# Performance work log

Measured on AMD Instinct MI355X. Metric: run time of the kernel, lower is better.

Reference implementation:

```python
import jax, jax.numpy as jnp
import numpy as np

NUM_HEADS = 4
CHUNK = 64
GATE_NORM = 16.0
EPS = 1e-5


def _xavier(key, fan_in, fan_out):
    gain = 2.0 ** (-2.5)
    limit = gain * np.sqrt(6.0 / (fan_in + fan_out))
    return jax.random.uniform(key, (fan_in, fan_out), jnp.float32, -limit, limit)


def setup_inputs() -> dict:
    key = jax.random.key(0)
    ks = jax.random.split(key, 8)
    B, L, D = 4, 2048, 1024
    Dk, Dv, R = 1024, 2048, 16
    x = jax.random.normal(ks[0], (B, L, D), jnp.float32)
    return {
        "x": x,
        "Wq": _xavier(ks[1], D, Dk),
        "Wk": _xavier(ks[2], D, Dk),
        "Wv": _xavier(ks[3], D, Dv),
        "Wg": _xavier(ks[4], D, Dv),
        "gk_w1": _xavier(ks[5], D, R),
        "gk_w2": _xavier(ks[6], R, Dk),
        "gk_b2": jnp.zeros((Dk,), jnp.float32),
        "g_norm_w": jnp.ones((Dv // NUM_HEADS,), jnp.float32),
        "Wo": _xavier(ks[7], Dv, D),
    }


def _to_chunks(t, B, H, NC, C):
    # [B,H,L,d] -> [NC,B,H,C,d]
    d = t.shape[-1]
    return t.reshape(B, H, NC, C, d).transpose(2, 0, 1, 3, 4)


def _gla_forward(x, Wq, Wk, Wv, Wg, gk_w1, gk_w2, gk_b2, g_norm_w, Wo):
    B, L, D = x.shape
    H = NUM_HEADS
    C = CHUNK
    NC = L // C

    q = x @ Wq  # [B,L,Dk]
    k = x @ Wk
    v = x @ Wv  # [B,L,Dv]
    gk = jax.nn.log_sigmoid((x @ gk_w1) @ gk_w2 + gk_b2) / GATE_NORM  # [B,L,Dk]

    def split_heads(t):
        return t.reshape(B, L, H, -1).transpose(0, 2, 1, 3)  # [B,H,L,d]

    q, k, v, gk = map(split_heads, (q, k, v, gk))
    dk = q.shape[-1]
    scale = dk ** -0.5

    qc = _to_chunks(q, B, H, NC, C)
    kc = _to_chunks(k, B, H, NC, C)
    vc = _to_chunks(v, B, H, NC, C)
    gc = _to_chunks(gk, B, H, NC, C)
    Bcum = jnp.cumsum(gc, axis=3)  # inclusive log-decay within chunk

    causal = jnp.tril(jnp.ones((C, C), jnp.float32))  # s <= t

    def step(Hst, inp):
        qi, ki, vi, bi = inp  # [B,H,C,dk/dv]
        qg = qi * jnp.exp(bi) * scale           # q_t * exp(B_t)
        kg = ki * jnp.exp(-bi)                  # k_s * exp(-B_s)
        o_inter = jnp.einsum('bhcd,bhde->bhce', qg, Hst)
        A = jnp.einsum('bhtd,bhsd->bhts', qg, kg) * causal
        o_intra = jnp.einsum('bhts,bhse->bhte', A, vi)
        b_last = bi[:, :, -1:, :]               # total chunk decay [B,H,1,dk]
        kH = ki * jnp.exp(b_last - bi)          # decay remaining after s
        H_new = jnp.exp(b_last).transpose(0, 1, 3, 2) * Hst + \
            jnp.einsum('bhcd,bhce->bhde', kH, vi)
        return H_new, o_inter + o_intra

    dv = v.shape[-1]
    H0 = jnp.zeros((B, H, dk, dv), jnp.float32)
    _, oc = jax.lax.scan(step, H0, (qc, kc, vc, Bcum))  # [NC,B,H,C,dv]
    o = oc.transpose(1, 2, 0, 3, 4).reshape(B, H, L, dv)
    o = o.transpose(0, 2, 1, 3)  # [B,L,H,dv]

    # FusedRMSNormSwishGate: RMSNorm(o) * w * swish(g)
    rms = jnp.sqrt(jnp.mean(o * o, axis=-1, keepdims=True) + EPS)
    o_n = (o / rms) * g_norm_w
    g = (x @ Wg).reshape(B, L, H, dv)
    o = o_n * g * jax.nn.sigmoid(g)
    return o.reshape(B, L, H * dv) @ Wo


def reference(x, Wq, Wk, Wv, Wg, gk_w1, gk_w2, gk_b2, g_norm_w, Wo):
    return _gla_forward(x, Wq, Wk, Wv, Wg, gk_w1, gk_w2, gk_b2, g_norm_w, Wo)
```

## Files before the change

kernel.cpp:

```cpp
#include <hip/hip_runtime.h>
#include <hip/hip_bf16.h>

typedef __attribute__((ext_vector_type(8))) __bf16 bf16x8;
typedef __attribute__((ext_vector_type(4))) __bf16 bf16x4;
typedef __attribute__((ext_vector_type(4))) float f32x4;

#define MFMA16(a, b, c) __builtin_amdgcn_mfma_f32_16x16x32_bf16((a), (b), (c), 0, 0, 0)

__device__ __forceinline__ void gload_lds16(const void* g, void* l) {
    __builtin_amdgcn_global_load_lds((const __attribute__((address_space(1))) void*)g,
                                     (__attribute__((address_space(3))) void*)l, 16, 0, 0);
}

__device__ __forceinline__ int lds_swz(int r, int ck) {
    int W = ((r & 15) << 6) | (ck << 4);
    W ^= ((W >> 7) & 7) << 4;
    return ((r >> 4) << 9) + (W >> 1);
}

__global__ __launch_bounds__(256) void cvt_bf16(const float* __restrict__ in,
                                                __bf16* __restrict__ out, int n4) {
    int i = blockIdx.x * 256 + threadIdx.x;
    if (i >= n4) return;
    f32x4 v = *(const f32x4*)(in + (size_t)i * 4);
    bf16x4 o;
#pragma unroll
    for (int j = 0; j < 4; j++) o[j] = (__bf16)v[j];
    *(bf16x4*)(out + (size_t)i * 4) = o;
}

__global__ __launch_bounds__(256) void transpose_w(const float* __restrict__ in,
                                                   __bf16* __restrict__ out, int R, int C) {
    __shared__ float tile[32][33];
    const int c0 = blockIdx.x * 32, r0 = blockIdx.y * 32;
    const int tx = threadIdx.x, ty = threadIdx.y;
#pragma unroll
    for (int k = 0; k < 32; k += 8)
        tile[ty + k][tx] = in[(size_t)(r0 + ty + k) * C + c0 + tx];
    __syncthreads();
#pragma unroll
    for (int k = 0; k < 32; k += 8)
        out[(size_t)(c0 + ty + k) * R + r0 + tx] = (__bf16)tile[tx][ty + k];
}

template <typename OUT_T>
__global__ __launch_bounds__(256) void gemm_bt(const __bf16* __restrict__ A,
                                               const __bf16* __restrict__ Bt,
                                               OUT_T* __restrict__ C, int M, int N, int K) {
    __shared__ alignas(16) __bf16 As[2][4096];
    __shared__ alignas(16) __bf16 Bs[2][4096];
    const int tid = threadIdx.x;
    const int wv = tid >> 6;
    const int l = tid & 63;
    const int nwg = gridDim.x;
    const int cpx = nwg >> 3;
    const int bid = blockIdx.x;
    const int wg = (bid & 7) * cpx + (bid >> 3);
    const int nbn = N >> 7;
    const int bm = wg / nbn, bn = wg - bm * nbn;

    const __bf16* Ab = A + (size_t)bm * 128 * K;
    const __bf16* Bb = Bt + (size_t)bn * 128 * K;
    const int L = (l << 4) ^ ((l >> 3) << 4);
    const int sr = L >> 6;
    const int sc8 = ((L >> 4) & 3) * 8;
    const int lr = tid & 15;
    const int ck = (tid >> 4) & 3;
    const int wm = (wv >> 1) * 64, wn = (wv & 1) * 64;

    auto STAGE = [&](int buf, int kt) {
        gload_lds16(Ab + (size_t)(wv * 16 + sr) * K + kt + sc8, &As[buf][0] + wv * 512);
        gload_lds16(Ab + (size_t)(64 + wv * 16 + sr) * K + kt + sc8, &As[buf][0] + 2048 + wv * 512);
        gload_lds16(Bb + (size_t)(wv * 16 + sr) * K + kt + sc8, &Bs[buf][0] + wv * 512);
        gload_lds16(Bb + (size_t)(64 + wv * 16 + sr) * K + kt + sc8, &Bs[buf][0] + 2048 + wv * 512);
    };

    const int nt = K >> 5;
    STAGE(0, 0);

    f32x4 acc[4][4] = {};
    for (int t = 0; t < nt; ++t) {
        __builtin_amdgcn_s_barrier();
        __builtin_amdgcn_sched_barrier(0);
        if (t + 1 < nt) {
            STAGE((t + 1) & 1, (t + 1) * 32);
            asm volatile("s_waitcnt vmcnt(4)" ::: "memory");
        } else {
            asm volatile("s_waitcnt vmcnt(0)" ::: "memory");
        }
        __builtin_amdgcn_sched_barrier(0);
        const __bf16* as = &As[t & 1][0];
        const __bf16* bs = &Bs[t & 1][0];
        bf16x8 af[4], bfr[4];
#pragma unroll
        for (int i = 0; i < 4; i++) af[i] = *(const bf16x8*)(as + lds_swz(wm + i * 16 + lr, ck));
#pragma unroll
        for (int j = 0; j < 4; j++) bfr[j] = *(const bf16x8*)(bs + lds_swz(wn + j * 16 + lr, ck));
#pragma unroll
        for (int i = 0; i < 4; i++)
#pragma unroll
            for (int j = 0; j < 4; j++) acc[i][j] = MFMA16(af[i], bfr[j], acc[i][j]);
        asm volatile("s_waitcnt lgkmcnt(0)" ::: "memory");
    }
    const int lro = ((tid >> 4) & 3) * 4;
#pragma unroll
    for (int i = 0; i < 4; i++)
#pragma unroll
        for (int j = 0; j < 4; j++) {
            size_t base = (size_t)(bm * 128 + wm + i * 16 + lro) * N + bn * 128 + wn + j * 16 + lr;
#pragma unroll
            for (int r = 0; r < 4; r++) C[base + (size_t)r * N] = (OUT_T)acc[i][j][r];
        }
}

__global__ __launch_bounds__(256) void gk1_proj(const float* __restrict__ x,
                                                const float* __restrict__ w1,
                                                float* __restrict__ t) {
    const int row = blockIdx.x * 4 + (threadIdx.x >> 6);
    const int l = threadIdx.x & 63;
    const int r = l & 15, kg = l >> 4;
    const float* xr = x + (size_t)row * 1024;
    const float* w1p = w1 + r;
    float acc = 0.f;
    for (int k = kg * 256; k < (kg + 1) * 256; ++k) acc = fmaf(xr[k], w1p[k * 16], acc);
    acc += __shfl_xor(acc, 16);
    acc += __shfl_xor(acc, 32);
    if (kg == 0) t[(size_t)row * 16 + r] = acc;
}

__global__ __launch_bounds__(1024, 4) void gate_qkg(
    const float* __restrict__ tbuf,
    const float* __restrict__ w2,
    const float* __restrict__ b2,
    const __bf16* __restrict__ qkbuf,
    __bf16* __restrict__ qg,
    __bf16* __restrict__ kg,
    __bf16* __restrict__ kgT,
    float* __restrict__ ebl)
{
    __shared__ alignas(16) float t_l[128 * 16];
    __shared__ float qs[4 * 256];
    __shared__ __bf16 kg_l[128 * 260];
    const int bid = blockIdx.x;
    const int bh = bid & 15, nc = bid >> 4;
    const int b = bh >> 2, h = bh & 3;
    const int tid = threadIdx.x;
    const int d = tid & 255, cq = tid >> 8;
    const int seq0 = b * 2048 + nc * 128;
    const int hd = h * 256 + d;

    for (int i = tid; i < 128 * 16; i += 1024) t_l[i] = tbuf[(size_t)seq0 * 16 + i];
    float w2c[16];
#pragma unroll
    for (int r = 0; r < 16; r++) w2c[r] = w2[r * 1024 + hd];
    const float b2v = b2[hd];
    __syncthreads();

    float bs[32];
    float run = 0.f;
#pragma unroll
    for (int j = 0; j < 32; j++) {
        const int c = cq * 32 + j;
        f32x4 t0 = *(const f32x4*)(t_l + c * 16);
        f32x4 t1 = *(const f32x4*)(t_l + c * 16 + 4);
        f32x4 t2 = *(const f32x4*)(t_l + c * 16 + 8);
        f32x4 t3 = *(const f32x4*)(t_l + c * 16 + 12);
        float u = b2v;
#pragma unroll
        for (int r = 0; r < 4; r++) {
            u = fmaf(t0[r], w2c[r], u);
            u = fmaf(t1[r], w2c[4 + r], u);
            u = fmaf(t2[r], w2c[8 + r], u);
            u = fmaf(t3[r], w2c[12 + r], u);
        }
        const float ls = fminf(u, 0.f) - __logf(1.f + __expf(-fabsf(u)));
        run += ls * 0.0625f;
        bs[j] = run;
    }
    qs[cq * 256 + d] = run;
    __syncthreads();

    float prefix = 0.f;
#pragma unroll
    for (int q = 0; q < 3; q++)
        if (q < cq) prefix += qs[q * 256 + d];

#pragma unroll
    for (int j = 0; j < 32; j++) {
        const int c = cq * 32 + j;
        const float bsum = prefix + bs[j];
        const float eb = __expf(bsum);
        const float en = __expf(-bsum);
        const float qv = (float)qkbuf[(size_t)(seq0 + c) * 2048 + hd];
        const float kv = (float)qkbuf[(size_t)(seq0 + c) * 2048 + 1024 + hd];
        qg[(size_t)(seq0 + c) * 1024 + hd] = (__bf16)(qv * eb * 0.0625f);
        const __bf16 kgv = (__bf16)(kv * en);
        kg[(size_t)(seq0 + c) * 1024 + hd] = kgv;
        kg_l[c * 260 + d] = kgv;
    }
    if (cq == 3) ebl[(size_t)(nc * 16 + bh) * 256 + d] = __expf(prefix + bs[31]);
    __syncthreads();

    {
        const int cc = tid & 127, dgroup = tid >> 7;
        for (int i = 0; i < 32; i++) {
            const int dd = dgroup * 32 + i;
            kgT[(size_t)(bh * 256 + dd) * 2048 + nc * 128 + cc] = kg_l[cc * 260 + dd];
        }
    }
}

__global__ __launch_bounds__(512) void a_mat(
    const __bf16* __restrict__ qg, const __bf16* __restrict__ kg,
    __bf16* __restrict__ Abuf) {
    const int pair = blockIdx.x;
    const int bh = pair & 15, nc = pair >> 4;
    const int b = bh >> 2, h = bh & 3;
    const int tid = threadIdx.x, wv = tid >> 6, l = tid & 63;
    const int lr = l & 15, lk = (l >> 4) * 8, lro = (l >> 4) * 4;
    const int seq0 = b * 2048 + nc * 128;
    __bf16* Ab = Abuf + (size_t)pair * 16384;

    {
        bf16x8 z = {};
        for (int i = tid; i < 2048; i += 512) *(bf16x8*)(Ab + (size_t)i * 8) = z;
    }
    __syncthreads();

    static const int TJ[36] = {0,1,1,2,2,2,3,3,3,3,4,4,4,4,4,5,5,5,5,5,5,
                               6,6,6,6,6,6,6,7,7,7,7,7,7,7,7};
    static const int TS[36] = {0,0,1,0,1,2,0,1,2,3,0,1,2,3,4,0,1,2,3,4,5,
                               0,1,2,3,4,5,6,0,1,2,3,4,5,6,7};
    for (int m = wv; m < 36; m += 8) {
        const int j = TJ[m], s = TS[m];
        f32x4 acc = {};
        const __bf16* qrow = qg + (size_t)(seq0 + j * 16 + lr) * 1024 + h * 256;
        const __bf16* krow = kg + (size_t)(seq0 + s * 16 + lr) * 1024 + h * 256;
#pragma unroll
        for (int ks = 0; ks < 8; ks++) {
            bf16x8 a = *(const bf16x8*)(qrow + ks * 32 + lk);
            bf16x8 bb = *(const bf16x8*)(krow + ks * 32 + lk);
            acc = MFMA16(a, bb, acc);
        }
#pragma unroll
        for (int r = 0; r < 4; r++) {
            const int t = j * 16 + lro + r;
            const int ss = s * 16 + lr;
            if (ss <= t) Ab[t * 128 + ss] = (__bf16)acc[r];
        }
    }
}

__global__ __launch_bounds__(256) void ointer(
    const __bf16* __restrict__ Abuf, const __bf16* __restrict__ qg,
    const __bf16* __restrict__ vt, const __bf16* __restrict__ UH,
    __bf16* __restrict__ ob) {
    __shared__ alignas(16) __bf16 As[2][4096];
    __shared__ alignas(16) __bf16 Bs[2][4096];
    const int tid = threadIdx.x;
    const int wv = tid >> 6;
    const int l = tid & 63;
    const int bid = blockIdx.x;
    const int wg = (bid & 7) * 128 + (bid >> 3);
    const int bn = wg & 3, pair = wg >> 2;
    const int bh = pair & 15, nc = pair >> 4;
    const int b = bh >> 2, h = bh & 3;
    const int seq0 = b * 2048 + nc * 128;
    const int L = (l << 4) ^ ((l >> 3) << 4);
    const int sr = L >> 6;
    const int sc8 = ((L >> 4) & 3) * 8;
    const int lr = tid & 15;
    const int ck = (tid >> 4) & 3;
    const int wm = (wv >> 1) * 64, wn = (wv & 1) * 64;
    const int KE = (nc == 0) ? 128 : 384;

    const __bf16* Ap = Abuf + (size_t)pair * 16384;
    const __bf16* Hb = UH + ((size_t)((nc - 1) * 16 + bh) * 512 + bn * 128) * 256;

    auto STAGE = [&](int buf, int kt) {
        const __bf16 *a0, *a1, *b0, *b1;
        if (kt < 128) {
            a0 = Ap + (size_t)(wv * 16 + sr) * 128 + kt + sc8;
            a1 = Ap + (size_t)(64 + wv * 16 + sr) * 128 + kt + sc8;
            b0 = vt + (size_t)(h * 512 + bn * 128 + wv * 16 + sr) * 8192 + seq0 + kt + sc8;
            b1 = vt + (size_t)(h * 512 + bn * 128 + 64 + wv * 16 + sr) * 8192 + seq0 + kt + sc8;
        } else {
            const int kd = kt - 128;
            a0 = qg + (size_t)(seq0 + wv * 16 + sr) * 1024 + h * 256 + kd + sc8;
            a1 = qg + (size_t)(seq0 + 64 + wv * 16 + sr) * 1024 + h * 256 + kd + sc8;
            b0 = Hb + (size_t)(wv * 16 + sr) * 256 + kd + sc8;
            b1 = Hb + (size_t)(64 + wv * 16 + sr) * 256 + kd + sc8;
        }
        gload_lds16(a0, &As[buf][0] + wv * 512);
        gload_lds16(a1, &As[buf][0] + 2048 + wv * 512);
        gload_lds16(b0, &Bs[buf][0] + wv * 512);
        gload_lds16(b1, &Bs[buf][0] + 2048 + wv * 512);
    };

    const int nt = KE >> 5;
    STAGE(0, 0);

    f32x4 acc[4][4] = {};
    for (int t = 0; t < nt; ++t) {
        __builtin_amdgcn_s_barrier();
        __builtin_amdgcn_sched_barrier(0);
        if (t + 1 < nt) {
            STAGE((t + 1) & 1, (t + 1) * 32);
            asm volatile("s_waitcnt vmcnt(4)" ::: "memory");
        } else {
            asm volatile("s_waitcnt vmcnt(0)" ::: "memory");
        }
        __builtin_amdgcn_sched_barrier(0);
        const __bf16* as = &As[t & 1][0];
        const __bf16* bs = &Bs[t & 1][0];
        bf16x8 af[4], bfr[4];
#pragma unroll
        for (int i = 0; i < 4; i++) af[i] = *(const bf16x8*)(as + lds_swz(wm + i * 16 + lr, ck));
#pragma unroll
        for (int j = 0; j < 4; j++) bfr[j] = *(const bf16x8*)(bs + lds_swz(wn + j * 16 + lr, ck));
#pragma unroll
        for (int i = 0; i < 4; i++)
#pragma unroll
            for (int j = 0; j < 4; j++) acc[i][j] = MFMA16(af[i], bfr[j], acc[i][j]);
        asm volatile("s_waitcnt lgkmcnt(0)" ::: "memory");
    }
    const int lro = ((tid >> 4) & 3) * 4;
#pragma unroll
    for (int i = 0; i < 4; i++)
#pragma unroll
        for (int j = 0; j < 4; j++) {
            size_t base = (size_t)(seq0 + wm + i * 16 + lro) * 2048 + h * 512 + bn * 128 + wn + j * 16 + lr;
#pragma unroll
            for (int r = 0; r < 4; r++) ob[base + (size_t)r * 2048] = (__bf16)acc[i][j][r];
        }
}

__global__ __launch_bounds__(512) void chunk_u(
    const __bf16* __restrict__ vt, const __bf16* __restrict__ kgT,
    __bf16* __restrict__ UH) {
    const int bid = blockIdx.x;
    const int bh = bid & 15, nc = (bid >> 4) & 15, q = bid >> 8;
    const int eh = q >> 1, dh = q & 1;
    const int b = bh >> 2, h = bh & 3;
    const int tid = threadIdx.x, wv = tid >> 6, l = tid & 63;
    const int lr = l & 15, lk = (l >> 4) * 8, lro = (l >> 4) * 4;
    const int seq0 = b * 2048 + nc * 128;
    const int e0 = eh * 256 + (wv >> 1) * 64;
    const int d0 = dh * 128 + (wv & 1) * 64;
    const __bf16* va = vt + (size_t)(h * 512 + e0) * 8192 + seq0;
    const __bf16* kb = kgT + (size_t)(bh * 256 + d0) * 2048 + nc * 128;

    f32x4 acc[4][4] = {};
#pragma unroll
    for (int ks = 0; ks < 4; ks++) {
        bf16x8 af[4], bf_[4];
#pragma unroll
        for (int i = 0; i < 4; i++)
            af[i] = *(const bf16x8*)(va + (size_t)(i * 16 + lr) * 8192 + ks * 32 + lk);
#pragma unroll
        for (int j = 0; j < 4; j++)
            bf_[j] = *(const bf16x8*)(kb + (size_t)(j * 16 + lr) * 2048 + ks * 32 + lk);
#pragma unroll
        for (int i = 0; i < 4; i++)
#pragma unroll
            for (int j = 0; j < 4; j++) acc[i][j] = MFMA16(af[i], bf_[j], acc[i][j]);
    }
    __bf16* ub = UH + ((size_t)(nc * 16 + bh) * 512 + e0) * 256 + d0;
#pragma unroll
    for (int i = 0; i < 4; i++)
#pragma unroll
        for (int j = 0; j < 4; j++)
#pragma unroll
            for (int r = 0; r < 4; r++)
                ub[(size_t)(i * 16 + lro + r) * 256 + j * 16 + lr] = (__bf16)acc[i][j][r];
}

__global__ __launch_bounds__(256) void hscan(__bf16* __restrict__ UH,
                                             const float* __restrict__ ebl) {
    const int t = blockIdx.x * 256 + threadIdx.x;
    const int bh = t >> 14;
    const int rem = t & 16383;
    const int e = rem >> 5, d0 = (rem & 31) * 8;
    float H[8];
#pragma unroll
    for (int j = 0; j < 8; j++) H[j] = 0.f;
    for (int i = 0; i < 16; i++) {
        size_t idx = ((size_t)(i * 16 + bh) * 512 + e) * 256 + d0;
        bf16x8 u = *(const bf16x8*)(UH + idx);
        const float* ep = ebl + (size_t)(i * 16 + bh) * 256 + d0;
        f32x4 e0v = *(const f32x4*)ep;
        f32x4 e1v = *(const f32x4*)(ep + 4);
        bf16x8 hw;
#pragma unroll
        for (int j = 0; j < 4; j++) {
            H[j] = e0v[j] * (H[j] + (float)u[j]);
            hw[j] = (__bf16)H[j];
        }
#pragma unroll
        for (int j = 4; j < 8; j++) {
            H[j] = e1v[j - 4] * (H[j] + (float)u[j]);
            hw[j] = (__bf16)H[j];
        }
        *(bf16x8*)(UH + idx) = hw;
    }
}

__global__ __launch_bounds__(256) void rms_gate(const __bf16* __restrict__ ob,
                                                const __bf16* __restrict__ gbuf,
                                                const float* __restrict__ gnw,
                                                __bf16* __restrict__ gated) {
    const int idx = blockIdx.x * 4 + (threadIdx.x >> 6);
    const int seq = idx >> 2, h = idx & 3;
    const int l = threadIdx.x & 63;
    bf16x8 o1 = *(const bf16x8*)(ob + (size_t)seq * 2048 + h * 512 + l * 8);
    float v[8];
    float ms = 0.f;
#pragma unroll
    for (int j = 0; j < 8; j++) {
        v[j] = (float)o1[j];
        ms += v[j] * v[j];
    }
#pragma unroll
    for (int off = 1; off < 64; off <<= 1) ms += __shfl_xor(ms, off);
    const float rinv = rsqrtf(ms * (1.f / 512.f) + 1e-5f);
    bf16x8 gv = *(const bf16x8*)(gbuf + (size_t)seq * 2048 + h * 512 + l * 8);
    const float* gw = gnw + l * 8;
    bf16x8 outv;
#pragma unroll
    for (int j = 0; j < 8; j++) {
        float g = (float)gv[j];
        float sig = 1.f / (1.f + expf(-g));
        outv[j] = (__bf16)(v[j] * rinv * gw[j] * g * sig);
    }
    *(bf16x8*)(gated + (size_t)seq * 2048 + h * 512 + l * 8) = outv;
}

extern "C" void kernel_launch(void* const* d_in, const int* in_sizes, int n_in,
                              void* d_out, int out_size, void* d_ws, size_t ws_size,
                              hipStream_t stream) {
    const float* x = (const float*)d_in[0];
    const float* Wq = (const float*)d_in[1];
    const float* Wk = (const float*)d_in[2];
    const float* Wv = (const float*)d_in[3];
    const float* Wg = (const float*)d_in[4];
    const float* w1 = (const float*)d_in[5];
    const float* w2 = (const float*)d_in[6];
    const float* b2 = (const float*)d_in[7];
    const float* gnw = (const float*)d_in[8];
    const float* Wo = (const float*)d_in[9];
    float* out = (float*)d_out;

    char* p = (char*)d_ws;
    auto nxt = [&](size_t bytes) {
        char* r = p;
        p += (bytes + 255) & ~(size_t)255;
        return r;
    };
    __bf16* xb = (__bf16*)nxt(8192ull * 1024 * 2);
    __bf16* WTqk = (__bf16*)nxt(2048ull * 1024 * 2);
    __bf16* WTg = (__bf16*)nxt(2048ull * 1024 * 2);
    __bf16* WvT = (__bf16*)nxt(2048ull * 1024 * 2);
    __bf16* WoT = (__bf16*)nxt(1024ull * 2048 * 2);
    __bf16* gbuf = (__bf16*)nxt(8192ull * 2048 * 2);
    __bf16* vt = (__bf16*)nxt(2048ull * 8192 * 2);
    float* tbuf = (float*)nxt(8192ull * 16 * 4);
    __bf16* qg = (__bf16*)nxt(8192ull * 1024 * 2);
    __bf16* kgT = (__bf16*)nxt(16ull * 256 * 2048 * 2);
    float* ebl = (float*)nxt(16ull * 16 * 256 * 4);
    __bf16* ob = (__bf16*)nxt(8192ull * 2048 * 2);
    __bf16* UH = (__bf16*)nxt(16ull * 16 * 512 * 256 * 2);
    __bf16* kg = xb;
    __bf16* qkbuf = UH;
    __bf16* gated = UH;
    __bf16* Abuf = WTqk;

    dim3 tb(32, 8);
    cvt_bf16<<<8192, 256, 0, stream>>>(x, xb, 2097152);
    transpose_w<<<dim3(32, 32), tb, 0, stream>>>(Wq, WTqk, 1024, 1024);
    transpose_w<<<dim3(32, 32), tb, 0, stream>>>(Wk, WTqk + 1024 * 1024, 1024, 1024);
    transpose_w<<<dim3(64, 32), tb, 0, stream>>>(Wg, WTg, 1024, 2048);
    transpose_w<<<dim3(64, 32), tb, 0, stream>>>(Wv, WvT, 1024, 2048);
    transpose_w<<<dim3(32, 64), tb, 0, stream>>>(Wo, WoT, 2048, 1024);
    gk1_proj<<<2048, 256, 0, stream>>>(x, w1, tbuf);
    gemm_bt<__bf16><<<1024, 256, 0, stream>>>(xb, WTqk, qkbuf, 8192, 2048, 1024);
    gemm_bt<__bf16><<<1024, 256, 0, stream>>>(xb, WTg, gbuf, 8192, 2048, 1024);
    gemm_bt<__bf16><<<1024, 256, 0, stream>>>(WvT, xb, vt, 2048, 8192, 1024);
    gate_qkg<<<256, 1024, 0, stream>>>(tbuf, w2, b2, qkbuf, qg, kg, kgT, ebl);
    a_mat<<<256, 512, 0, stream>>>(qg, kg, Abuf);
    chunk_u<<<1024, 512, 0, stream>>>(vt, kgT, UH);
    hscan<<<1024, 256, 0, stream>>>(UH, ebl);
    ointer<<<1024, 256, 0, stream>>>(Abuf, qg, vt, UH, ob);
    rms_gate<<<8192, 256, 0, stream>>>(ob, gbuf, gnw, gated);
    gemm_bt<float><<<512, 256, 0, stream>>>(gated, WoT, out, 8192, 1024, 2048);
}
```

Measured before the change: 411.2 us.

## Enlarge GEMM tiles to 256x256 with 8 waves and interleaved K-stage loading

Rewrites the shared bf16 GEMM to use 256x256 output tiles, 512 threads (8 waves) and a K-step of 64 with a new LDS swizzle. The next stage's loads are spread across four sub-steps between MFMA groups, and s_setprio is raised around the MFMA bursts. The aim is more data reuse per tile and better overlap of loads with compute. In exchange, the grid for the projection GEMMs drops to 256 and 128 workgroups, which can leave compute units idle on a large GPU. LDS use per block also rises to 128KB, limiting occupancy.

```diff
diff --git a/kernel.cpp b/kernel.cpp
--- a/kernel.cpp
+++ b/kernel.cpp
@@ -16,6 +16,13 @@
     int W = ((r & 15) << 6) | (ck << 4);
     W ^= ((W >> 7) & 7) << 4;
     return ((r >> 4) << 9) + (W >> 1);
+}
+
+__device__ __forceinline__ int swz64(int row, int cb) {
+    int off = (row << 7) | cb;
+    int W = off & 2047;
+    W ^= ((W >> 8) & 7) << 4;
+    return (((off & ~2047) | W) >> 1);
 }
 
 __global__ __launch_bounds__(256) void cvt_bf16(const float* __restrict__ in,
@@ -44,72 +51,89 @@
 }
 
 template <typename OUT_T>
-__global__ __launch_bounds__(256) void gemm_bt(const __bf16* __restrict__ A,
-                                               const __bf16* __restrict__ Bt,
-                                               OUT_T* __restrict__ C, int M, int N, int K) {
-    __shared__ alignas(16) __bf16 As[2][4096];
-    __shared__ alignas(16) __bf16 Bs[2][4096];
+__global__ __launch_bounds__(512, 2) void gemm_bt(const __bf16* __restrict__ A,
+                                                  const __bf16* __restrict__ Bt,
+                                                  OUT_T* __restrict__ C, int M, int N, int K) {
+    __shared__ alignas(16) __bf16 As[2][16384];
+    __shared__ alignas(16) __bf16 Bs[2][16384];
     const int tid = threadIdx.x;
-    const int wv = tid >> 6;
-    const int l = tid & 63;
-    const int nwg = gridDim.x;
-    const int cpx = nwg >> 3;
-    const int bid = blockIdx.x;
+    const int wv = tid >> 6, l = tid & 63;
+    const int nwg = gridDim.x, cpx = nwg >> 3, bid = blockIdx.x;
     const int wg = (bid & 7) * cpx + (bid >> 3);
-    const int nbn = N >> 7;
+    const int nbn = N >> 8;
     const int bm = wg / nbn, bn = wg - bm * nbn;
-
-    const __bf16* Ab = A + (size_t)bm * 128 * K;
-    const __bf16* Bb = Bt + (size_t)bn * 128 * K;
-    const int L = (l << 4) ^ ((l >> 3) << 4);
-    const int sr = L >> 6;
-    const int sc8 = ((L >> 4) & 3) * 8;
-    const int lr = tid & 15;
-    const int ck = (tid >> 4) & 3;
-    const int wm = (wv >> 1) * 64, wn = (wv & 1) * 64;
-
-    auto STAGE = [&](int buf, int kt) {
-        gload_lds16(Ab + (size_t)(wv * 16 + sr) * K + kt + sc8, &As[buf][0] + wv * 512);
-        gload_lds16(Ab + (size_t)(64 + wv * 16 + sr) * K + kt + sc8, &As[buf][0] + 2048 + wv * 512);
-        gload_lds16(Bb + (size_t)(wv * 16 + sr) * K + kt + sc8, &Bs[buf][0] + wv * 512);
-        gload_lds16(Bb + (size_t)(64 + wv * 16 + sr) * K + kt + sc8, &Bs[buf][0] + 2048 + wv * 512);
+    const __bf16* Ab = A + (size_t)bm * 256 * K;
+    const __bf16* Bb = Bt + (size_t)bn * 256 * K;
+    const int wr = wv >> 2, wc = wv & 3;
+    const int lr = l & 15, kg = l >> 4;
+
+    const int offw = wv * 1024 + l * 16;
+    const int Wb = offw & 2047;
+    const int Lsb = Wb ^ (((Wb >> 8) & 7) << 4);
+    const int srow_u = (offw >> 11) * 16 + (Lsb >> 7);
+    const int scol = (Lsb & 127) >> 1;
+
+    auto STAGE2 = [&](int buf, int kt, int u) {
+        gload_lds16(Ab + (size_t)(u * 64 + srow_u) * K + kt + scol,
+                    &As[buf][0] + u * 4096 + wv * 512);
+        gload_lds16(Bb + (size_t)(u * 64 + srow_u) * K + kt + scol,
+                    &Bs[buf][0] + u * 4096 + wv * 512);
     };
 
-    const int nt = K >> 5;
-    STAGE(0, 0);
-
-    f32x4 acc[4][4] = {};
+    const int nt = K >> 6;
+#pragma unroll
+    for (int u = 0; u < 4; ++u) STAGE2(0, 0, u);
+
+    f32x4 acc[8][4] = {};
     for (int t = 0; t < nt; ++t) {
+        const int R = t & 1;
+        asm volatile("s_waitcnt vmcnt(0)" ::: "memory");
         __builtin_amdgcn_s_barrier();
         __builtin_amdgcn_sched_barrier(0);
-        if (t + 1 < nt) {
-            STAGE((t + 1) & 1, (t + 1) * 32);
-            asm volatile("s_waitcnt vmcnt(4)" ::: "memory");
-        } else {
-            asm volatile("s_waitcnt vmcnt(0)" ::: "memory");
-        }
-        __builtin_amdgcn_sched_barrier(0);
-        const __bf16* as = &As[t & 1][0];
-        const __bf16* bs = &Bs[t & 1][0];
-        bf16x8 af[4], bfr[4];
-#pragma unroll
-        for (int i = 0; i < 4; i++) af[i] = *(const bf16x8*)(as + lds_swz(wm + i * 16 + lr, ck));
-#pragma unroll
-        for (int j = 0; j < 4; j++) bfr[j] = *(const bf16x8*)(bs + lds_swz(wn + j * 16 + lr, ck));
-#pragma unroll
-        for (int i = 0; i < 4; i++)
-#pragma unroll
-            for (int j = 0; j < 4; j++) acc[i][j] = MFMA16(af[i], bfr[j], acc[i][j]);
-        asm volatile("s_waitcnt lgkmcnt(0)" ::: "memory");
-    }
-    const int lro = ((tid >> 4) & 3) * 4;
-#pragma unroll
-    for (int i = 0; i < 4; i++)
-#pragma unroll
-        for (int j = 0; j < 4; j++) {
-            size_t base = (size_t)(bm * 128 + wm + i * 16 + lro) * N + bn * 128 + wn + j * 16 + lr;
-#pragma unroll
-            for (int r = 0; r < 4; r++) C[base + (size_t)r * N] = (OUT_T)acc[i][j][r];
+        const __bf16* as = &As[R][0];
+        const __bf16* bs = &Bs[R][0];
+        bf16x8 bF[4][2];
+#pragma unroll
+        for (int q = 0; q < 4; ++q) {
+            if (t + 1 < nt) STAGE2(1 - R, (t + 1) * 64, q);
+            if (q == 0) {
+#pragma unroll
+                for (int j = 0; j < 4; ++j)
+#pragma unroll
+                    for (int ks = 0; ks < 2; ++ks)
+                        bF[j][ks] = *(const bf16x8*)(bs + swz64(wc * 64 + j * 16 + lr,
+                                                                ks * 64 + kg * 16));
+            }
+            bf16x8 aF[2][2];
+#pragma unroll
+            for (int tt = 0; tt < 2; ++tt)
+#pragma unroll
+                for (int ks = 0; ks < 2; ++ks)
+                    aF[tt][ks] = *(const bf16x8*)(as + swz64(wr * 128 + (q * 2 + tt) * 16 + lr,
+                                                             ks * 64 + kg * 16));
+            asm volatile("s_waitcnt lgkmcnt(0)" ::: "memory");
+            __builtin_amdgcn_sched_barrier(0);
+            __builtin_amdgcn_s_setprio(1);
+#pragma unroll
+            for (int tt = 0; tt < 2; ++tt)
+#pragma unroll
+                for (int j = 0; j < 4; ++j)
+#pragma unroll
+                    for (int ks = 0; ks < 2; ++ks)
+                        acc[q * 2 + tt][j] = MFMA16(aF[tt][ks], bF[j][ks], acc[q * 2 + tt][j]);
+            __builtin_amdgcn_s_setprio(0);
+            __builtin_amdgcn_s_barrier();
+        }
+    }
+    const int lro = kg * 4;
+#pragma unroll
+    for (int i = 0; i < 8; ++i)
+#pragma unroll
+        for (int j = 0; j < 4; ++j) {
+            size_t base = (size_t)(bm * 256 + wr * 128 + i * 16 + lro) * N +
+                          bn * 256 + wc * 64 + j * 16 + lr;
+#pragma unroll
+            for (int r = 0; r < 4; ++r) C[base + (size_t)r * N] = (OUT_T)acc[i][j][r];
         }
 }
 
@@ -129,15 +153,10 @@
 }
 
 __global__ __launch_bounds__(1024, 4) void gate_qkg(
-    const float* __restrict__ tbuf,
-    const float* __restrict__ w2,
-    const float* __restrict__ b2,
-    const __bf16* __restrict__ qkbuf,
-    __bf16* __restrict__ qg,
-    __bf16* __restrict__ kg,
-    __bf16* __restrict__ kgT,
-    float* __restrict__ ebl)
-{
+    const float* __restrict__ tbuf, const float* __restrict__ w2,
+    const float* __restrict__ b2, const __bf16* __restrict__ qkbuf,
+    __bf16* __restrict__ qg, __bf16* __restrict__ kg,
+    __bf16* __restrict__ kgT, float* __restrict__ ebl) {
     __shared__ alignas(16) float t_l[128 * 16];
     __shared__ float qs[4 * 256];
     __shared__ __bf16 kg_l[128 * 260];
@@ -482,14 +501,14 @@
     transpose_w<<<dim3(64, 32), tb, 0, stream>>>(Wv, WvT, 1024, 2048);
     transpose_w<<<dim3(32, 64), tb, 0, stream>>>(Wo, WoT, 2048, 1024);
     gk1_proj<<<2048, 256, 0, stream>>>(x, w1, tbuf);
-    gemm_bt<__bf16><<<1024, 256, 0, stream>>>(xb, WTqk, qkbuf, 8192, 2048, 1024);
-    gemm_bt<__bf16><<<1024, 256, 0, stream>>>(xb, WTg, gbuf, 8192, 2048, 1024);
-    gemm_bt<__bf16><<<1024, 256, 0, stream>>>(WvT, xb, vt, 2048, 8192, 1024);
+    gemm_bt<__bf16><<<256, 512, 0, stream>>>(xb, WTqk, qkbuf, 8192, 2048, 1024);
+    gemm_bt<__bf16><<<256, 512, 0, stream>>>(xb, WTg, gbuf, 8192, 2048, 1024);
+    gemm_bt<__bf16><<<256, 512, 0, stream>>>(WvT, xb, vt, 2048, 8192, 1024);
     gate_qkg<<<256, 1024, 0, stream>>>(tbuf, w2, b2, qkbuf, qg, kg, kgT, ebl);
     a_mat<<<256, 512, 0, stream>>>(qg, kg, Abuf);
     chunk_u<<<1024, 512, 0, stream>>>(vt, kgT, UH);
     hscan<<<1024, 256, 0, stream>>>(UH, ebl);
     ointer<<<1024, 256, 0, stream>>>(Abuf, qg, vt, UH, ob);
     rms_gate<<<8192, 256, 0, stream>>>(ob, gbuf, gnw, gated);
-    gemm_bt<float><<<512, 256, 0, stream>>>(gated, WoT, out, 8192, 1024, 2048);
-}
+    gemm_bt<float><<<128, 512, 0, stream>>>(gated, WoT, out, 8192, 1024, 2048);
+}
```

Result: slower. 464.3 us (+12.9%).
